# Kernel tuning notes

Hardware: AMD Instinct MI355X
Metric: run time of the kernel (lower is better)

Reference implementation:

```python
import jax, jax.numpy as jnp
import numpy as np

B, M, N_DIM = 2048, 1024, 64


def setup_inputs() -> dict:
    key = jax.random.key(0)
    ks = jax.random.split(key, 6)
    X = jax.random.normal(ks[0], (B, N_DIM), dtype=jnp.float32)
    Mu0 = jax.random.normal(ks[1], (M, N_DIM), dtype=jnp.float32)
    Mu1 = jax.random.normal(ks[2], (M, N_DIM), dtype=jnp.float32)
    # diagonal variances must be positive
    S0 = jax.random.uniform(ks[3], (M, N_DIM), dtype=jnp.float32, minval=0.1, maxval=1.0)
    S1 = jax.random.uniform(ks[4], (M, N_DIM), dtype=jnp.float32, minval=0.1, maxval=1.0)
    Lam = jax.random.uniform(ks[5], (M,), dtype=jnp.float32, minval=0.01, maxval=1.0)
    Lam = Lam / jnp.sum(Lam)  # transport-plan weights sum to 1
    return {"X": X, "Mu0": Mu0, "Mu1": Mu1, "S0": S0, "S1": S1,
            "Lam": Lam, "t": 0.3, "epsilon": 0.5}


def reference(X, Mu0, Mu1, S0, S1, Lam, t, epsilon):
    # GMMflow_fast.calc_u with sparse coupling of M nonzero (i,j) pairs.
    eps2 = epsilon ** 2
    Ds = jnp.sqrt(4.0 * S0 * S1 + epsilon ** 4)            # [M, n]
    Cs = 0.5 * (Ds - eps2)                                  # [M, n]
    v = Mu1 - Mu0                                           # [M, n]
    Mut = (1.0 - t) * Mu0 + t * Mu1                         # [M, n]
    Sigma = ((1.0 - t) ** 2) * S0 + (t ** 2) * S1 + 2.0 * t * (1.0 - t) * (Cs + 0.5 * eps2)
    Pt = t * S1 + (1.0 - t) * Cs
    Qt = (1.0 - t) * S0 + t * Cs
    St = Pt - Qt - eps2 * t
    K = St / Sigma                                          # [M, n]

    Xd = X[:, None, :] - Mut[None, :, :]                    # [B, M, n]
    U = K[None, :, :] * Xd + v[None, :, :]                  # [B, M, n]

    # Gaussian log-prob plus (n/2) log(2*pi), matching the torch code:
    # log N(x; mu, Sigma) + n/2 log(2pi) = -0.5 * sum(d^2/Sigma + log Sigma)
    logw = -0.5 * jnp.sum(Xd * Xd / Sigma[None, :, :] + jnp.log(Sigma)[None, :, :], axis=-1)  # [B, M]
    logw = jnp.clip(logw, -50.0, 50.0)
    W = jnp.exp(logw) * Lam[None, :]                        # [B, M]

    u = jnp.einsum('bm,bmd->bd', W, U)                      # [B, n]
    norm = jnp.sum(W, axis=1, keepdims=True)                # [B, 1]
    return u / norm
```

## Files before the change

### kernel.cpp

```cpp
#include <hip/hip_runtime.h>
#include <math.h>


#define B_N 2048
#define M_N 1024
#define NSPLIT 16
#define BT 64
#define MS 64
#define PROW 132

__global__ __launch_bounds__(256)
void prep_kernel(const float* __restrict__ X,
                 const float* __restrict__ Mu0, const float* __restrict__ Mu1,
                 const float* __restrict__ S0, const float* __restrict__ S1,
                 const float* __restrict__ T, const float* __restrict__ E,
                 float2* __restrict__ wsAP, float2* __restrict__ wsKG,
                 float* __restrict__ qArr, float* __restrict__ XT) {
    __shared__ __align__(16) float sT[64 * 68];
    const int tid = threadIdx.x;
    if (blockIdx.x < 256) {
        int gid = blockIdx.x * 256 + tid;
        int m = gid >> 6, d = gid & 63;
        float t = T[0], e = E[0];
        float eps2 = e * e, eps4 = eps2 * eps2;
        int idx = m * 64 + d;
        float s0 = S0[idx], s1 = S1[idx];
        float mu0 = Mu0[idx], mu1 = Mu1[idx];
        float Ds = sqrtf(4.f * s0 * s1 + eps4);
        float Cs = 0.5f * (Ds - eps2);
        float omt = 1.f - t;
        float sig = omt * omt * s0 + t * t * s1 + 2.f * t * omt * (Cs + 0.5f * eps2);
        float St = (t * s1 + omt * Cs) - (omt * s0 + t * Cs) - eps2 * t;
        float a = 1.f / sig;
        float K = St * a;
        float mut = omt * mu0 + t * mu1;
        wsAP[idx] = make_float2(a, -2.f * mut * a);
        wsKG[idx] = make_float2(K, (mu1 - mu0) - K * mut);
        float qd = mut * mut * a + logf(sig);
        #pragma unroll
        for (int off = 32; off > 0; off >>= 1) qd += __shfl_xor(qd, off, 64);
        if (d == 0) qArr[m] = qd;
    } else {
        int Boff = (blockIdx.x - 256) * 64;
        const float4* X4 = (const float4*)X;
        #pragma unroll
        for (int it = 0; it < 4; it++) {
            int i = it * 256 + tid;
            int b = i >> 4, dq = i & 15;
            float4 v = X4[(Boff + b) * 16 + dq];
            sT[(4 * dq + 0) * 68 + b] = v.x;
            sT[(4 * dq + 1) * 68 + b] = v.y;
            sT[(4 * dq + 2) * 68 + b] = v.z;
            sT[(4 * dq + 3) * 68 + b] = v.w;
        }
        __syncthreads();
        float4* XT4 = (float4*)XT;
        #pragma unroll
        for (int it = 0; it < 4; it++) {
            int i = it * 256 + tid;
            int d = i >> 4, bq = i & 15;
            XT4[d * (B_N / 4) + (Boff >> 2) + bq] = *(const float4*)&sT[d * 68 + 4 * bq];
        }
    }
}

__global__ __launch_bounds__(256, 2)
void gmm_main_kernel(const float* __restrict__ Lam,
                     const float2* __restrict__ wsAP, const float2* __restrict__ wsKG,
                     const float* __restrict__ XT, const float* __restrict__ qArr,
                     float* __restrict__ part) {
    __shared__ __align__(16) float smem[17280];
    float* sX = smem;
    float* sA = smem + 4096;
    float* sP = smem + 8448;
    float* sW = smem + 12800;
    float* sQ = smem + 17152;
    float* sL = smem + 17216;

    const int tid  = threadIdx.x;
    const int Boff = blockIdx.x * BT;
    const int Moff = blockIdx.y * MS;
    const int mg = tid & 15;
    const int bq = tid >> 4;

    {
        const float4* src = (const float4*)XT;
        float4* dst = (float4*)sX;
        #pragma unroll
        for (int it = 0; it < 4; it++) {
            int i = it * 256 + tid;
            int d = i >> 4, b4 = i & 15;
            dst[d * 16 + b4] = src[d * (B_N / 4) + (Boff >> 2) + b4];
        }
    }
    {
        const float4* srcAP = (const float4*)wsAP;
        #pragma unroll
        for (int it = 0; it < 8; it++) {
            int i = it * 256 + tid;
            int m = i >> 5, dp = i & 31;
            float4 v = srcAP[(Moff + m) * 32 + dp];
            int d = 2 * dp;
            sA[d * 68 + m] = v.x;  sP[d * 68 + m] = v.y;
            sA[(d + 1) * 68 + m] = v.z;  sP[(d + 1) * 68 + m] = v.w;
        }
        if (tid < 64) sQ[tid] = qArr[Moff + tid];
        else if (tid < 128) sL[tid - 64] = Lam[Moff + tid - 64];
    }
    __syncthreads();

    float acc[4][4];
    #pragma unroll
    for (int j = 0; j < 4; j++)
        #pragma unroll
        for (int i = 0; i < 4; i++) acc[j][i] = 0.f;
    {
        const float4* sX4 = (const float4*)sX;
        #pragma unroll 4
        for (int d = 0; d < 64; d++) {
            float4 xv = sX4[d * 16 + bq];
            float4 a4 = *(const float4*)&sA[d * 68 + 4 * mg];
            float4 p4 = *(const float4*)&sP[d * 68 + 4 * mg];
            float xs[4] = {xv.x, xv.y, xv.z, xv.w};
            float as[4] = {a4.x, a4.y, a4.z, a4.w};
            float ps[4] = {p4.x, p4.y, p4.z, p4.w};
            #pragma unroll
            for (int j = 0; j < 4; j++) {
                float xj = xs[j];
                #pragma unroll
                for (int i = 0; i < 4; i++)
                    acc[j][i] = fmaf(xj, fmaf(xj, as[i], ps[i]), acc[j][i]);
            }
        }
    }

    {
        #pragma unroll
        for (int i = 0; i < 4; i++) {
            int m = 4 * mg + i;
            float q = sQ[m], lam = sL[m];
            float4 wv;
            float lw0 = fminf(50.f, fmaxf(-50.f, -0.5f * (acc[0][i] + q)));
            float lw1 = fminf(50.f, fmaxf(-50.f, -0.5f * (acc[1][i] + q)));
            float lw2 = fminf(50.f, fmaxf(-50.f, -0.5f * (acc[2][i] + q)));
            float lw3 = fminf(50.f, fmaxf(-50.f, -0.5f * (acc[3][i] + q)));
            wv.x = __expf(lw0) * lam;
            wv.y = __expf(lw1) * lam;
            wv.z = __expf(lw2) * lam;
            wv.w = __expf(lw3) * lam;
            *(float4*)&sW[m * 68 + 4 * bq] = wv;
        }
    }
    __syncthreads();

    float s1a[4][4], s2a[4][4], nb[4];
    #pragma unroll
    for (int j = 0; j < 4; j++) {
        nb[j] = 0.f;
        #pragma unroll
        for (int k = 0; k < 4; k++) { s1a[j][k] = 0.f; s2a[j][k] = 0.f; }
    }
    {
        const float4* KG4 = (const float4*)wsKG;
        #pragma unroll 4
        for (int m = 0; m < MS; m++) {
            float4 wv  = *(const float4*)&sW[m * 68 + 4 * bq];
            float4 kgA = KG4[(Moff + m) * 32 + 2 * mg];
            float4 kgB = KG4[(Moff + m) * 32 + 2 * mg + 1];
            float ws4[4] = {wv.x, wv.y, wv.z, wv.w};
            #pragma unroll
            for (int j = 0; j < 4; j++) {
                float wj = ws4[j];
                s1a[j][0] = fmaf(wj, kgA.x, s1a[j][0]);
                s2a[j][0] = fmaf(wj, kgA.y, s2a[j][0]);
                s1a[j][1] = fmaf(wj, kgA.z, s1a[j][1]);
                s2a[j][1] = fmaf(wj, kgA.w, s2a[j][1]);
                s1a[j][2] = fmaf(wj, kgB.x, s1a[j][2]);
                s2a[j][2] = fmaf(wj, kgB.y, s2a[j][2]);
                s1a[j][3] = fmaf(wj, kgB.z, s1a[j][3]);
                s2a[j][3] = fmaf(wj, kgB.w, s2a[j][3]);
                nb[j] += wj;
            }
        }
    }

    {
        int d0 = 4 * mg;
        #pragma unroll
        for (int j = 0; j < 4; j++) {
            int b = Boff + 4 * bq + j;
            float* row = part + ((size_t)blockIdx.y * B_N + b) * PROW;
            *(float4*)(row + d0)      = make_float4(s1a[j][0], s1a[j][1], s1a[j][2], s1a[j][3]);
            *(float4*)(row + 64 + d0) = make_float4(s2a[j][0], s2a[j][1], s2a[j][2], s2a[j][3]);
            if (mg == 0) row[128] = nb[j];
        }
    }
}

__global__ __launch_bounds__(256)
void finalize_kernel(const float* __restrict__ X, const float* __restrict__ part,
                     float* __restrict__ out) {
    int gid = blockIdx.x * 256 + threadIdx.x;
    int b = gid >> 6, d = gid & 63;
    float a1 = 0.f, a2 = 0.f, nn = 0.f;
    #pragma unroll
    for (int s = 0; s < NSPLIT; s++) {
        const float* row = part + ((size_t)s * B_N + b) * PROW;
        a1 += row[d];
        a2 += row[64 + d];
        nn += row[128];
    }
    out[gid] = (X[gid] * a1 + a2) / nn;
}

extern "C" void kernel_launch(void* const* d_in, const int* in_sizes, int n_in,
                              void* d_out, int out_size, void* d_ws, size_t ws_size,
                              hipStream_t stream) {
    (void)in_sizes; (void)n_in; (void)out_size; (void)ws_size;
    const float* X   = (const float*)d_in[0];
    const float* Mu0 = (const float*)d_in[1];
    const float* Mu1 = (const float*)d_in[2];
    const float* S0  = (const float*)d_in[3];
    const float* S1  = (const float*)d_in[4];
    const float* Lam = (const float*)d_in[5];
    const float* T   = (const float*)d_in[6];
    const float* E   = (const float*)d_in[7];

    char* ws = (char*)d_ws;
    float2* wsAP = (float2*)(ws);
    float2* wsKG = (float2*)(ws + (512 << 10));
    float*  wsXT = (float*)(ws + (1 << 20));
    float*  qArr = (float*)(ws + (1 << 20) + (512 << 10));
    float*  part = (float*)(ws + (1 << 20) + (512 << 10) + 4096);

    prep_kernel<<<288, 256, 0, stream>>>(X, Mu0, Mu1, S0, S1, T, E, wsAP, wsKG, qArr, wsXT);
    dim3 grid(B_N / BT, NSPLIT);
    gmm_main_kernel<<<grid, 256, 0, stream>>>(Lam, wsAP, wsKG, wsXT, qArr, part);
    finalize_kernel<<<512, 256, 0, stream>>>(X, part, (float*)d_out);
}
```

Baseline: 98.27 us.

## Double batch tile to 128 and stage KG coefficients in shared memory

The batch tile per block grows from 64 to 128 rows, so each thread computes 8x4 outputs instead of 4x4 and reuses each loaded A/P/KG value across twice as many batch rows. The KG coefficients are now loaded cooperatively into shared memory, aliased over the X region after a new barrier, instead of being read from global memory inside the accumulation loop. Per-block work doubles while the grid halves to 16x16=256 blocks, and launch bounds drop to one block per SM, which lowers occupancy and latency hiding in exchange for higher arithmetic intensity.

```diff
diff --git a/kernel.cpp b/kernel.cpp
--- a/kernel.cpp
+++ b/kernel.cpp
@@ -5,7 +5,7 @@
 #define B_N 2048
 #define M_N 1024
 #define NSPLIT 16
-#define BT 64
+#define BT 128
 #define MS 64
 #define PROW 132
 
@@ -64,33 +64,34 @@
     }
 }
 
-__global__ __launch_bounds__(256, 2)
+__global__ __launch_bounds__(256, 1)
 void gmm_main_kernel(const float* __restrict__ Lam,
                      const float2* __restrict__ wsAP, const float2* __restrict__ wsKG,
                      const float* __restrict__ XT, const float* __restrict__ qArr,
                      float* __restrict__ part) {
-    __shared__ __align__(16) float smem[17280];
-    float* sX = smem;
-    float* sA = smem + 4096;
-    float* sP = smem + 8448;
-    float* sW = smem + 12800;
-    float* sQ = smem + 17152;
-    float* sL = smem + 17216;
+    __shared__ __align__(16) float smem[17024];
+    float* sX  = smem;
+    float* sA  = smem + 8192;
+    float* sP  = smem + 12544;
+    float* sKG = smem;
+    float* sW  = smem + 8192;
+    float* sQ  = smem + 16896;
+    float* sL  = smem + 16960;
 
     const int tid  = threadIdx.x;
     const int Boff = blockIdx.x * BT;
     const int Moff = blockIdx.y * MS;
+    const int bg = tid >> 4;
     const int mg = tid & 15;
-    const int bq = tid >> 4;
-
-    {
-        const float4* src = (const float4*)XT;
+
+    {
+        const float4* XT4 = (const float4*)XT;
         float4* dst = (float4*)sX;
         #pragma unroll
-        for (int it = 0; it < 4; it++) {
-            int i = it * 256 + tid;
-            int d = i >> 4, b4 = i & 15;
-            dst[d * 16 + b4] = src[d * (B_N / 4) + (Boff >> 2) + b4];
+        for (int it = 0; it < 8; it++) {
+            int i = it * 256 + tid;
+            int d = i >> 5, q = i & 31;
+            dst[d * 32 + q] = XT4[d * (B_N / 4) + (Boff >> 2) + q];
         }
     }
     {
@@ -109,23 +110,26 @@
     }
     __syncthreads();
 
-    float acc[4][4];
+    float acc[8][4];
     #pragma unroll
-    for (int j = 0; j < 4; j++)
+    for (int j = 0; j < 8; j++)
         #pragma unroll
         for (int i = 0; i < 4; i++) acc[j][i] = 0.f;
     {
         const float4* sX4 = (const float4*)sX;
+        const float4* sA4 = (const float4*)sA;
+        const float4* sP4 = (const float4*)sP;
         #pragma unroll 4
         for (int d = 0; d < 64; d++) {
-            float4 xv = sX4[d * 16 + bq];
-            float4 a4 = *(const float4*)&sA[d * 68 + 4 * mg];
-            float4 p4 = *(const float4*)&sP[d * 68 + 4 * mg];
-            float xs[4] = {xv.x, xv.y, xv.z, xv.w};
+            float4 xA = sX4[d * 32 + 2 * bg];
+            float4 xB = sX4[d * 32 + 2 * bg + 1];
+            float4 a4 = sA4[d * 17 + mg];
+            float4 p4 = sP4[d * 17 + mg];
+            float xs[8] = {xA.x, xA.y, xA.z, xA.w, xB.x, xB.y, xB.z, xB.w};
             float as[4] = {a4.x, a4.y, a4.z, a4.w};
             float ps[4] = {p4.x, p4.y, p4.z, p4.w};
             #pragma unroll
-            for (int j = 0; j < 4; j++) {
+            for (int j = 0; j < 8; j++) {
                 float xj = xs[j];
                 #pragma unroll
                 for (int i = 0; i < 4; i++)
@@ -133,44 +137,57 @@
             }
         }
     }
-
-    {
+    __syncthreads();
+
+    {
+        const float4* KG4 = (const float4*)wsKG;
+        float4* sKG4 = (float4*)sKG;
+        float4 tmp[8];
+        #pragma unroll
+        for (int it = 0; it < 8; it++) {
+            int i = it * 256 + tid;
+            tmp[it] = KG4[(size_t)(Moff + (i >> 5)) * 32 + (i & 31)];
+        }
         #pragma unroll
         for (int i = 0; i < 4; i++) {
             int m = 4 * mg + i;
             float q = sQ[m], lam = sL[m];
-            float4 wv;
-            float lw0 = fminf(50.f, fmaxf(-50.f, -0.5f * (acc[0][i] + q)));
-            float lw1 = fminf(50.f, fmaxf(-50.f, -0.5f * (acc[1][i] + q)));
-            float lw2 = fminf(50.f, fmaxf(-50.f, -0.5f * (acc[2][i] + q)));
-            float lw3 = fminf(50.f, fmaxf(-50.f, -0.5f * (acc[3][i] + q)));
-            wv.x = __expf(lw0) * lam;
-            wv.y = __expf(lw1) * lam;
-            wv.z = __expf(lw2) * lam;
-            wv.w = __expf(lw3) * lam;
-            *(float4*)&sW[m * 68 + 4 * bq] = wv;
+            float w[8];
+            #pragma unroll
+            for (int j = 0; j < 8; j++) {
+                float lw = fminf(50.f, fmaxf(-50.f, -0.5f * (acc[j][i] + q)));
+                w[j] = __expf(lw) * lam;
+            }
+            *(float4*)&sW[m * 132 + 8 * bg]     = make_float4(w[0], w[1], w[2], w[3]);
+            *(float4*)&sW[m * 132 + 8 * bg + 4] = make_float4(w[4], w[5], w[6], w[7]);
+        }
+        #pragma unroll
+        for (int it = 0; it < 8; it++) {
+            int i = it * 256 + tid;
+            sKG4[(i >> 5) * 32 + (i & 31)] = tmp[it];
         }
     }
     __syncthreads();
 
-    float s1a[4][4], s2a[4][4], nb[4];
+    float s1a[8][4], s2a[8][4], nb[8];
     #pragma unroll
-    for (int j = 0; j < 4; j++) {
+    for (int j = 0; j < 8; j++) {
         nb[j] = 0.f;
         #pragma unroll
         for (int k = 0; k < 4; k++) { s1a[j][k] = 0.f; s2a[j][k] = 0.f; }
     }
     {
-        const float4* KG4 = (const float4*)wsKG;
+        const float4* sKG4 = (const float4*)sKG;
         #pragma unroll 4
         for (int m = 0; m < MS; m++) {
-            float4 wv  = *(const float4*)&sW[m * 68 + 4 * bq];
-            float4 kgA = KG4[(Moff + m) * 32 + 2 * mg];
-            float4 kgB = KG4[(Moff + m) * 32 + 2 * mg + 1];
-            float ws4[4] = {wv.x, wv.y, wv.z, wv.w};
+            float4 wv1 = *(const float4*)&sW[m * 132 + 8 * bg];
+            float4 wv2 = *(const float4*)&sW[m * 132 + 8 * bg + 4];
+            float4 kgA = sKG4[m * 32 + 2 * mg];
+            float4 kgB = sKG4[m * 32 + 2 * mg + 1];
+            float ws8[8] = {wv1.x, wv1.y, wv1.z, wv1.w, wv2.x, wv2.y, wv2.z, wv2.w};
             #pragma unroll
-            for (int j = 0; j < 4; j++) {
-                float wj = ws4[j];
+            for (int j = 0; j < 8; j++) {
+                float wj = ws8[j];
                 s1a[j][0] = fmaf(wj, kgA.x, s1a[j][0]);
                 s2a[j][0] = fmaf(wj, kgA.y, s2a[j][0]);
                 s1a[j][1] = fmaf(wj, kgA.z, s1a[j][1]);
@@ -187,8 +204,8 @@
     {
         int d0 = 4 * mg;
         #pragma unroll
-        for (int j = 0; j < 4; j++) {
-            int b = Boff + 4 * bq + j;
+        for (int j = 0; j < 8; j++) {
+            int b = Boff + 8 * bg + j;
             float* row = part + ((size_t)blockIdx.y * B_N + b) * PROW;
             *(float4*)(row + d0)      = make_float4(s1a[j][0], s1a[j][1], s1a[j][2], s1a[j][3]);
             *(float4*)(row + 64 + d0) = make_float4(s2a[j][0], s2a[j][1], s2a[j][2], s2a[j][3]);
```

Result: no change. 98.16 us (-0.1%).

## Move both GMM contractions to bf16 MFMA with split hi/lo precision

Applied to the files above, without the earlier changes.

Both inner contractions, the quadratic log-weight form and the weighted sum over components, are recast as matrix multiplies. They run on MFMA 16x16x32 bf16 instructions, using a three-term hi/lo bf16 split to keep accuracy close to fp32. The prep kernel now emits the bf16 hi/lo operand matrices, including a ones row for the normaliser. The batch tile doubles to 128 with one block per CU. This trades FP32 VALU FMAs for matrix-core throughput, at the cost of extra prep traffic, a bigger LDS footprint, lower occupancy, and some precision risk.

```diff
diff --git a/kernel.cpp b/kernel.cpp
--- a/kernel.cpp
+++ b/kernel.cpp
@@ -5,195 +5,262 @@
 #define B_N 2048
 #define M_N 1024
 #define NSPLIT 16
-#define BT 64
+#define BT 128
 #define MS 64
 #define PROW 132
+
+typedef short bf16x8 __attribute__((ext_vector_type(8)));
+typedef float f32x4 __attribute__((ext_vector_type(4)));
+
+static __device__ __forceinline__ unsigned short bf16rn(float f) {
+    union { float f; unsigned u; } v; v.f = f;
+    unsigned r = v.u + 0x7FFF + ((v.u >> 16) & 1);
+    return (unsigned short)(r >> 16);
+}
+static __device__ __forceinline__ float bf2f(unsigned short h) {
+    union { unsigned u; float f; } v; v.u = ((unsigned)h) << 16;
+    return v.f;
+}
 
 __global__ __launch_bounds__(256)
 void prep_kernel(const float* __restrict__ X,
                  const float* __restrict__ Mu0, const float* __restrict__ Mu1,
                  const float* __restrict__ S0, const float* __restrict__ S1,
                  const float* __restrict__ T, const float* __restrict__ E,
-                 float2* __restrict__ wsAP, float2* __restrict__ wsKG,
-                 float* __restrict__ qArr, float* __restrict__ XT) {
-    __shared__ __align__(16) float sT[64 * 68];
+                 unsigned short* __restrict__ A1h, unsigned short* __restrict__ A1l,
+                 unsigned short* __restrict__ B1h, unsigned short* __restrict__ B1l,
+                 unsigned short* __restrict__ VTh, unsigned short* __restrict__ VTl,
+                 float* __restrict__ qArr) {
     const int tid = threadIdx.x;
-    if (blockIdx.x < 256) {
-        int gid = blockIdx.x * 256 + tid;
-        int m = gid >> 6, d = gid & 63;
-        float t = T[0], e = E[0];
-        float eps2 = e * e, eps4 = eps2 * eps2;
-        int idx = m * 64 + d;
-        float s0 = S0[idx], s1 = S1[idx];
-        float mu0 = Mu0[idx], mu1 = Mu1[idx];
-        float Ds = sqrtf(4.f * s0 * s1 + eps4);
-        float Cs = 0.5f * (Ds - eps2);
-        float omt = 1.f - t;
-        float sig = omt * omt * s0 + t * t * s1 + 2.f * t * omt * (Cs + 0.5f * eps2);
-        float St = (t * s1 + omt * Cs) - (omt * s0 + t * Cs) - eps2 * t;
-        float a = 1.f / sig;
-        float K = St * a;
-        float mut = omt * mu0 + t * mu1;
-        wsAP[idx] = make_float2(a, -2.f * mut * a);
-        wsKG[idx] = make_float2(K, (mu1 - mu0) - K * mut);
-        float qd = mut * mut * a + logf(sig);
-        #pragma unroll
-        for (int off = 32; off > 0; off >>= 1) qd += __shfl_xor(qd, off, 64);
-        if (d == 0) qArr[m] = qd;
+    if (blockIdx.x < 16) {
+        __shared__ float sKf[64 * 65];
+        __shared__ float sGf[64 * 65];
+        const int m0 = blockIdx.x * 64;
+        const float t = T[0], e = E[0];
+        const float eps2 = e * e, eps4 = eps2 * eps2, omt = 1.f - t;
+        const int d = tid & 63;
+        #pragma unroll 4
+        for (int it = 0; it < 16; it++) {
+            int mi = it * 4 + (tid >> 6);
+            int m = m0 + mi;
+            int idx = m * 64 + d;
+            float s0 = S0[idx], s1 = S1[idx];
+            float mu0 = Mu0[idx], mu1 = Mu1[idx];
+            float Ds = sqrtf(4.f * s0 * s1 + eps4);
+            float Cs = 0.5f * (Ds - eps2);
+            float sig = omt * omt * s0 + t * t * s1 + 2.f * t * omt * (Cs + 0.5f * eps2);
+            float St = (t * s1 + omt * Cs) - (omt * s0 + t * Cs) - eps2 * t;
+            float a = 1.f / sig;
+            float K = St * a;
+            float mut = omt * mu0 + t * mu1;
+            float pp = -2.f * mut * a;
+            float g = (mu1 - mu0) - K * mut;
+            unsigned short ah = bf16rn(a);
+            B1h[m * 128 + d] = ah;
+            B1l[m * 128 + d] = bf16rn(a - bf2f(ah));
+            unsigned short ph = bf16rn(pp);
+            B1h[m * 128 + 64 + d] = ph;
+            B1l[m * 128 + 64 + d] = bf16rn(pp - bf2f(ph));
+            sKf[mi * 65 + d] = K;
+            sGf[mi * 65 + d] = g;
+            float qd = mut * mut * a + logf(sig);
+            #pragma unroll
+            for (int off = 32; off > 0; off >>= 1) qd += __shfl_xor(qd, off, 64);
+            if (d == 0) qArr[m] = qd;
+        }
+        __syncthreads();
+        #pragma unroll 4
+        for (int it = 0; it < 32; it++) {
+            int i = it * 256 + tid;
+            int n = i >> 6, mm = i & 63;
+            float v = (n < 64) ? sKf[mm * 65 + n] : sGf[mm * 65 + (n - 64)];
+            unsigned short h = bf16rn(v);
+            VTh[n * 1024 + m0 + mm] = h;
+            VTl[n * 1024 + m0 + mm] = bf16rn(v - bf2f(h));
+        }
+    } else if (blockIdx.x < 528) {
+        int gid = (blockIdx.x - 16) * 256 + tid;
+        int b = gid >> 6, d = gid & 63;
+        float x = X[gid];
+        float y = x * x;
+        unsigned short yh = bf16rn(y);
+        A1h[b * 128 + d] = yh;
+        A1l[b * 128 + d] = bf16rn(y - bf2f(yh));
+        unsigned short xh = bf16rn(x);
+        A1h[b * 128 + 64 + d] = xh;
+        A1l[b * 128 + 64 + d] = bf16rn(x - bf2f(xh));
     } else {
-        int Boff = (blockIdx.x - 256) * 64;
-        const float4* X4 = (const float4*)X;
         #pragma unroll
         for (int it = 0; it < 4; it++) {
-            int i = it * 256 + tid;
-            int b = i >> 4, dq = i & 15;
-            float4 v = X4[(Boff + b) * 16 + dq];
-            sT[(4 * dq + 0) * 68 + b] = v.x;
-            sT[(4 * dq + 1) * 68 + b] = v.y;
-            sT[(4 * dq + 2) * 68 + b] = v.z;
-            sT[(4 * dq + 3) * 68 + b] = v.w;
-        }
-        __syncthreads();
-        float4* XT4 = (float4*)XT;
-        #pragma unroll
-        for (int it = 0; it < 4; it++) {
-            int i = it * 256 + tid;
-            int d = i >> 4, bq = i & 15;
-            XT4[d * (B_N / 4) + (Boff >> 2) + bq] = *(const float4*)&sT[d * 68 + 4 * bq];
-        }
-    }
-}
-
-__global__ __launch_bounds__(256, 2)
+            int m = it * 256 + tid;
+            VTh[128 * 1024 + m] = 0x3F80;
+            VTl[128 * 1024 + m] = 0;
+        }
+    }
+}
+
+__global__ __launch_bounds__(256, 1)
 void gmm_main_kernel(const float* __restrict__ Lam,
-                     const float2* __restrict__ wsAP, const float2* __restrict__ wsKG,
-                     const float* __restrict__ XT, const float* __restrict__ qArr,
-                     float* __restrict__ part) {
-    __shared__ __align__(16) float smem[17280];
-    float* sX = smem;
-    float* sA = smem + 4096;
-    float* sP = smem + 8448;
-    float* sW = smem + 12800;
-    float* sQ = smem + 17152;
-    float* sL = smem + 17216;
+                     const unsigned short* __restrict__ A1h, const unsigned short* __restrict__ A1l,
+                     const unsigned short* __restrict__ B1h, const unsigned short* __restrict__ B1l,
+                     const unsigned short* __restrict__ VTh, const unsigned short* __restrict__ VTl,
+                     const float* __restrict__ qArr, float* __restrict__ part) {
+    __shared__ __align__(16) char smem_raw[104960];
+    unsigned short* sm = (unsigned short*)smem_raw;
+    unsigned short* sA1h = sm;
+    unsigned short* sA1l = sm + 17408;
+    unsigned short* sVh  = sm;
+    unsigned short* sVl  = sm + 10368;
+    unsigned short* sB1h = sm + 34816;
+    unsigned short* sB1l = sm + 43520;
+    unsigned short* sWh  = sm + 34816;
+    unsigned short* sWl  = sm + 43520;
+    float* sQ = (float*)(smem_raw + 104448);
+    float* sL = (float*)(smem_raw + 104704);
 
     const int tid  = threadIdx.x;
     const int Boff = blockIdx.x * BT;
     const int Moff = blockIdx.y * MS;
-    const int mg = tid & 15;
-    const int bq = tid >> 4;
-
-    {
-        const float4* src = (const float4*)XT;
-        float4* dst = (float4*)sX;
+    const int w    = tid >> 6;
+    const int lane = tid & 63;
+    const int c = lane & 15, q = lane >> 4;
+
+    {
+        const float4* gAh = (const float4*)A1h + (size_t)Boff * 16;
+        const float4* gAl = (const float4*)A1l + (size_t)Boff * 16;
+        #pragma unroll
+        for (int it = 0; it < 8; it++) {
+            int i = it * 256 + tid;
+            int row = i >> 4, cc = i & 15;
+            *(float4*)(sA1h + row * 136 + cc * 8) = gAh[row * 16 + cc];
+            *(float4*)(sA1l + row * 136 + cc * 8) = gAl[row * 16 + cc];
+        }
+        const float4* gBh = (const float4*)B1h + (size_t)Moff * 16;
+        const float4* gBl = (const float4*)B1l + (size_t)Moff * 16;
         #pragma unroll
         for (int it = 0; it < 4; it++) {
             int i = it * 256 + tid;
-            int d = i >> 4, b4 = i & 15;
-            dst[d * 16 + b4] = src[d * (B_N / 4) + (Boff >> 2) + b4];
-        }
-    }
-    {
-        const float4* srcAP = (const float4*)wsAP;
-        #pragma unroll
-        for (int it = 0; it < 8; it++) {
-            int i = it * 256 + tid;
-            int m = i >> 5, dp = i & 31;
-            float4 v = srcAP[(Moff + m) * 32 + dp];
-            int d = 2 * dp;
-            sA[d * 68 + m] = v.x;  sP[d * 68 + m] = v.y;
-            sA[(d + 1) * 68 + m] = v.z;  sP[(d + 1) * 68 + m] = v.w;
+            int row = i >> 4, cc = i & 15;
+            *(float4*)(sB1h + row * 136 + cc * 8) = gBh[row * 16 + cc];
+            *(float4*)(sB1l + row * 136 + cc * 8) = gBl[row * 16 + cc];
         }
         if (tid < 64) sQ[tid] = qArr[Moff + tid];
         else if (tid < 128) sL[tid - 64] = Lam[Moff + tid - 64];
     }
     __syncthreads();
 
-    float acc[4][4];
+    f32x4 acc1[2][4];
     #pragma unroll
-    for (int j = 0; j < 4; j++)
-        #pragma unroll
-        for (int i = 0; i < 4; i++) acc[j][i] = 0.f;
-    {
-        const float4* sX4 = (const float4*)sX;
-        #pragma unroll 4
-        for (int d = 0; d < 64; d++) {
-            float4 xv = sX4[d * 16 + bq];
-            float4 a4 = *(const float4*)&sA[d * 68 + 4 * mg];
-            float4 p4 = *(const float4*)&sP[d * 68 + 4 * mg];
-            float xs[4] = {xv.x, xv.y, xv.z, xv.w};
-            float as[4] = {a4.x, a4.y, a4.z, a4.w};
-            float ps[4] = {p4.x, p4.y, p4.z, p4.w};
+    for (int i = 0; i < 2; i++)
+        #pragma unroll
+        for (int j = 0; j < 4; j++) acc1[i][j] = (f32x4){0.f, 0.f, 0.f, 0.f};
+    {
+        #pragma unroll
+        for (int ks = 0; ks < 4; ks++) {
+            bf16x8 Ah[2], Al[2], Bh[4], Bl[4];
+            #pragma unroll
+            for (int i = 0; i < 2; i++) {
+                int row = (2 * w + i) * 16 + c;
+                Ah[i] = *(const bf16x8*)(sA1h + row * 136 + ks * 32 + q * 8);
+                Al[i] = *(const bf16x8*)(sA1l + row * 136 + ks * 32 + q * 8);
+            }
             #pragma unroll
             for (int j = 0; j < 4; j++) {
-                float xj = xs[j];
+                int row = j * 16 + c;
+                Bh[j] = *(const bf16x8*)(sB1h + row * 136 + ks * 32 + q * 8);
+                Bl[j] = *(const bf16x8*)(sB1l + row * 136 + ks * 32 + q * 8);
+            }
+            #pragma unroll
+            for (int i = 0; i < 2; i++)
                 #pragma unroll
-                for (int i = 0; i < 4; i++)
-                    acc[j][i] = fmaf(xj, fmaf(xj, as[i], ps[i]), acc[j][i]);
-            }
-        }
-    }
-
-    {
-        #pragma unroll
-        for (int i = 0; i < 4; i++) {
-            int m = 4 * mg + i;
-            float q = sQ[m], lam = sL[m];
-            float4 wv;
-            float lw0 = fminf(50.f, fmaxf(-50.f, -0.5f * (acc[0][i] + q)));
-            float lw1 = fminf(50.f, fmaxf(-50.f, -0.5f * (acc[1][i] + q)));
-            float lw2 = fminf(50.f, fmaxf(-50.f, -0.5f * (acc[2][i] + q)));
-            float lw3 = fminf(50.f, fmaxf(-50.f, -0.5f * (acc[3][i] + q)));
-            wv.x = __expf(lw0) * lam;
-            wv.y = __expf(lw1) * lam;
-            wv.z = __expf(lw2) * lam;
-            wv.w = __expf(lw3) * lam;
-            *(float4*)&sW[m * 68 + 4 * bq] = wv;
+                for (int j = 0; j < 4; j++) {
+                    acc1[i][j] = __builtin_amdgcn_mfma_f32_16x16x32_bf16(Ah[i], Bh[j], acc1[i][j], 0, 0, 0);
+                    acc1[i][j] = __builtin_amdgcn_mfma_f32_16x16x32_bf16(Ah[i], Bl[j], acc1[i][j], 0, 0, 0);
+                    acc1[i][j] = __builtin_amdgcn_mfma_f32_16x16x32_bf16(Al[i], Bh[j], acc1[i][j], 0, 0, 0);
+                }
         }
     }
     __syncthreads();
 
-    float s1a[4][4], s2a[4][4], nb[4];
+    {
+        const float4* gVh = (const float4*)VTh;
+        const float4* gVl = (const float4*)VTl;
+        int mo8 = Moff >> 3;
+        #pragma unroll
+        for (int it = 0; it < 5; it++) {
+            int i = it * 256 + tid;
+            if (i < 1152) {
+                int row = i >> 3, cc = i & 7;
+                *(float4*)(sVh + row * 72 + cc * 8) = gVh[row * 128 + mo8 + cc];
+                *(float4*)(sVl + row * 72 + cc * 8) = gVl[row * 128 + mo8 + cc];
+            }
+        }
+        #pragma unroll
+        for (int i = 0; i < 2; i++)
+            #pragma unroll
+            for (int j = 0; j < 4; j++) {
+                int m = j * 16 + c;
+                float qm = sQ[m], lm = sL[m];
+                #pragma unroll
+                for (int r = 0; r < 4; r++) {
+                    int bl = (2 * w + i) * 16 + q * 4 + r;
+                    float lw = -0.5f * (acc1[i][j][r] + qm);
+                    lw = fminf(50.f, fmaxf(-50.f, lw));
+                    float wf = __expf(lw) * lm;
+                    unsigned short wh = bf16rn(wf);
+                    sWh[bl * 68 + m] = wh;
+                    sWl[bl * 68 + m] = bf16rn(wf - bf2f(wh));
+                }
+            }
+    }
+    __syncthreads();
+
+    f32x4 acc2[2][9];
     #pragma unroll
-    for (int j = 0; j < 4; j++) {
-        nb[j] = 0.f;
-        #pragma unroll
-        for (int k = 0; k < 4; k++) { s1a[j][k] = 0.f; s2a[j][k] = 0.f; }
-    }
-    {
-        const float4* KG4 = (const float4*)wsKG;
-        #pragma unroll 4
-        for (int m = 0; m < MS; m++) {
-            float4 wv  = *(const float4*)&sW[m * 68 + 4 * bq];
-            float4 kgA = KG4[(Moff + m) * 32 + 2 * mg];
-            float4 kgB = KG4[(Moff + m) * 32 + 2 * mg + 1];
-            float ws4[4] = {wv.x, wv.y, wv.z, wv.w};
-            #pragma unroll
-            for (int j = 0; j < 4; j++) {
-                float wj = ws4[j];
-                s1a[j][0] = fmaf(wj, kgA.x, s1a[j][0]);
-                s2a[j][0] = fmaf(wj, kgA.y, s2a[j][0]);
-                s1a[j][1] = fmaf(wj, kgA.z, s1a[j][1]);
-                s2a[j][1] = fmaf(wj, kgA.w, s2a[j][1]);
-                s1a[j][2] = fmaf(wj, kgB.x, s1a[j][2]);
-                s2a[j][2] = fmaf(wj, kgB.y, s2a[j][2]);
-                s1a[j][3] = fmaf(wj, kgB.z, s1a[j][3]);
-                s2a[j][3] = fmaf(wj, kgB.w, s2a[j][3]);
-                nb[j] += wj;
-            }
-        }
-    }
-
-    {
-        int d0 = 4 * mg;
-        #pragma unroll
-        for (int j = 0; j < 4; j++) {
-            int b = Boff + 4 * bq + j;
-            float* row = part + ((size_t)blockIdx.y * B_N + b) * PROW;
-            *(float4*)(row + d0)      = make_float4(s1a[j][0], s1a[j][1], s1a[j][2], s1a[j][3]);
-            *(float4*)(row + 64 + d0) = make_float4(s2a[j][0], s2a[j][1], s2a[j][2], s2a[j][3]);
-            if (mg == 0) row[128] = nb[j];
-        }
+    for (int i = 0; i < 2; i++)
+        #pragma unroll
+        for (int j = 0; j < 9; j++) acc2[i][j] = (f32x4){0.f, 0.f, 0.f, 0.f};
+    {
+        #pragma unroll
+        for (int ks = 0; ks < 2; ks++) {
+            bf16x8 Wh[2], Wl[2], Vh[9], Vl[9];
+            #pragma unroll
+            for (int i = 0; i < 2; i++) {
+                int row = (2 * w + i) * 16 + c;
+                Wh[i] = *(const bf16x8*)(sWh + row * 68 + ks * 32 + q * 8);
+                Wl[i] = *(const bf16x8*)(sWl + row * 68 + ks * 32 + q * 8);
+            }
+            #pragma unroll
+            for (int j = 0; j < 9; j++) {
+                int row = j * 16 + c;
+                Vh[j] = *(const bf16x8*)(sVh + row * 72 + ks * 32 + q * 8);
+                Vl[j] = *(const bf16x8*)(sVl + row * 72 + ks * 32 + q * 8);
+            }
+            #pragma unroll
+            for (int i = 0; i < 2; i++)
+                #pragma unroll
+                for (int j = 0; j < 9; j++) {
+                    acc2[i][j] = __builtin_amdgcn_mfma_f32_16x16x32_bf16(Wh[i], Vh[j], acc2[i][j], 0, 0, 0);
+                    acc2[i][j] = __builtin_amdgcn_mfma_f32_16x16x32_bf16(Wh[i], Vl[j], acc2[i][j], 0, 0, 0);
+                    acc2[i][j] = __builtin_amdgcn_mfma_f32_16x16x32_bf16(Wl[i], Vh[j], acc2[i][j], 0, 0, 0);
+                }
+        }
+    }
+
+    {
+        #pragma unroll
+        for (int i = 0; i < 2; i++)
+            #pragma unroll
+            for (int j = 0; j < 9; j++) {
+                #pragma unroll
+                for (int r = 0; r < 4; r++) {
+                    int bl = (2 * w + i) * 16 + q * 4 + r;
+                    int n = j * 16 + c;
+                    float* row = part + ((size_t)blockIdx.y * B_N + Boff + bl) * PROW;
+                    if (j < 8) row[n] = acc2[i][j][r];
+                    else if (c == 0) row[128] = acc2[i][j][r];
+                }
+            }
     }
 }
 
@@ -227,14 +294,18 @@
     const float* E   = (const float*)d_in[7];
 
     char* ws = (char*)d_ws;
-    float2* wsAP = (float2*)(ws);
-    float2* wsKG = (float2*)(ws + (512 << 10));
-    float*  wsXT = (float*)(ws + (1 << 20));
-    float*  qArr = (float*)(ws + (1 << 20) + (512 << 10));
-    float*  part = (float*)(ws + (1 << 20) + (512 << 10) + 4096);
-
-    prep_kernel<<<288, 256, 0, stream>>>(X, Mu0, Mu1, S0, S1, T, E, wsAP, wsKG, qArr, wsXT);
+    unsigned short* A1h = (unsigned short*)(ws);
+    unsigned short* A1l = (unsigned short*)(ws + 524288);
+    unsigned short* B1h = (unsigned short*)(ws + 1048576);
+    unsigned short* B1l = (unsigned short*)(ws + 1310720);
+    unsigned short* VTh = (unsigned short*)(ws + 1572864);
+    unsigned short* VTl = (unsigned short*)(ws + 1867776);
+    float* qArr = (float*)(ws + 2162688);
+    float* part = (float*)(ws + 2166784);
+
+    prep_kernel<<<529, 256, 0, stream>>>(X, Mu0, Mu1, S0, S1, T, E,
+                                         A1h, A1l, B1h, B1l, VTh, VTl, qArr);
     dim3 grid(B_N / BT, NSPLIT);
-    gmm_main_kernel<<<grid, 256, 0, stream>>>(Lam, wsAP, wsKG, wsXT, qArr, part);
+    gmm_main_kernel<<<grid, 256, 0, stream>>>(Lam, A1h, A1l, B1h, B1l, VTh, VTl, qArr, part);
     finalize_kernel<<<512, 256, 0, stream>>>(X, part, (float*)d_out);
 }
```

Result: slower. 103.5 us (+5.3%).
